# Kernel tuning notes

Hardware: AMD Instinct MI355X
Metric: run time of the kernel (lower is better)

The kernel has to match this reference:

```python
import jax, jax.numpy as jnp
import numpy as np

D = 768   # embedding_len
NL = 4    # nleft attributes
NR = 4    # nright attributes
LL = 256  # total left tokens
LR = 256  # total right tokens
DE = (NL + NR) * D  # entity-matching highway width


def setup_inputs() -> dict:
    key = jax.random.key(0)
    ks = jax.random.split(key, 12)
    f = lambda k, s: (jax.random.normal(k, s, jnp.float32) * 0.02)
    return {
        "left_emb": jax.random.normal(ks[0], (LL, D), jnp.float32),
        "right_emb": jax.random.normal(ks[1], (LR, D), jnp.float32),
        "Wn_tok": f(ks[2], (D, D)), "bn_tok": jnp.zeros((D,), jnp.float32),
        "Wg_tok": f(ks[3], (D, D)), "bg_tok": jnp.full((D,), -2.0, jnp.float32),
        "W_lin_tok": f(ks[4], (D, 1)), "b_lin_tok": jnp.zeros((1,), jnp.float32),
        "attr_emb_left": f(ks[5], (NL, D)),
        "attr_emb_right": f(ks[6], (NR, D)),
        "Wn_ent": f(ks[7], (DE, DE)), "bn_ent": jnp.zeros((DE,), jnp.float32),
        "Wg_ent": f(ks[8], (DE, DE)), "bg_ent": jnp.full((DE,), -2.0, jnp.float32),
        "W_lin_ent": f(ks[9], (DE, 2)), "b_lin_ent": jnp.zeros((2,), jnp.float32),
        "empty_attr_res": f(ks[10], (D,)),
        # per-attribute token counts; left includes an empty attribute
        "left_attrs_len": jnp.array([100, 80, 76, 0], dtype=jnp.int32),
        "right_attrs_len": jnp.array([64, 64, 64, 64], dtype=jnp.int32),
    }


def _highway(x, Wn, bn, Wg, bg):
    h = jax.nn.relu(x @ Wn + bn)
    g = jax.nn.sigmoid(x @ Wg + bg)
    return h * g + (1.0 - g) * x


def _token_matching(left, right, Wn, bn, Wg, bg, W_lin, b_lin):
    # compare_matrix: [L_left, L_right, D]
    cmp = jnp.abs(left[:, None, :] - right[None, :, :])
    hw = _highway(cmp, Wn, bn, Wg, bg)
    scores = hw @ W_lin + b_lin                     # [Ll, Lr, 1]
    # softmax over dim=1 (right tokens); only argmax is used downstream
    idx = jnp.argmax(scores[..., 0], axis=1)        # [Ll]
    return jnp.take_along_axis(cmp, idx[:, None, None], axis=1)[:, 0, :]  # [Ll, D]


def _attribute_matching(tokens, field_emb, cmp_res, lens, empty_attr):
    # ragged per-attribute softmax-weighted segment reduction
    n = field_emb.shape[0]
    L = tokens.shape[0]
    seg = jnp.repeat(jnp.arange(n), lens, total_repeat_length=L)   # [L]
    scores = jnp.einsum('ld,ld->l', tokens, field_emb[seg])        # [L]
    m = jax.ops.segment_max(scores, seg, num_segments=n)
    e = jnp.exp(scores - m[seg])
    z = jax.ops.segment_sum(e, seg, num_segments=n)
    w = e / z[seg]                                                  # softmax within segment
    reps = jax.ops.segment_sum(w[:, None] * cmp_res, seg, num_segments=n)  # [n, D]
    return jnp.where(lens[:, None] > 0, reps, empty_attr[None, :])


def reference(left_emb, right_emb, Wn_tok, bn_tok, Wg_tok, bg_tok,
              W_lin_tok, b_lin_tok, attr_emb_left, attr_emb_right,
              Wn_ent, bn_ent, Wg_ent, bg_ent, W_lin_ent, b_lin_ent,
              empty_attr_res, left_attrs_len, right_attrs_len):
    left_cmp = _token_matching(left_emb, right_emb, Wn_tok, bn_tok, Wg_tok, bg_tok,
                               W_lin_tok, b_lin_tok)
    right_cmp = _token_matching(right_emb, left_emb, Wn_tok, bn_tok, Wg_tok, bg_tok,
                                W_lin_tok, b_lin_tok)
    left_rep = _attribute_matching(left_emb, attr_emb_left, left_cmp,
                                   left_attrs_len, empty_attr_res)
    right_rep = _attribute_matching(right_emb, attr_emb_right, right_cmp,
                                    right_attrs_len, empty_attr_res)
    concat = jnp.concatenate([left_rep, right_rep], axis=0).reshape(1, -1)  # [1, DE]
    hw = _highway(concat, Wn_ent, bn_ent, Wg_ent, bg_ent)
    logits = hw @ W_lin_ent + b_lin_ent                                     # [1, 2]
    return jax.nn.softmax(logits, axis=1).flatten()                         # [2]
```

## Files before the change

### kernel.cpp

```cpp
#include <hip/hip_runtime.h>
#include <math.h>
#include <stdint.h>

#define DD 768
#define NT 256
#define DE 6144

typedef _Float16 half8 __attribute__((ext_vector_type(8)));
typedef _Float16 half4 __attribute__((ext_vector_type(4)));
typedef short short8 __attribute__((ext_vector_type(8)));
typedef float floatx4 __attribute__((ext_vector_type(4)));

__device__ __forceinline__ void async_ld16(const void* g, void* l) {
  __builtin_amdgcn_global_load_lds(
      (const __attribute__((address_space(1))) unsigned int*)g,
      (__attribute__((address_space(3))) unsigned int*)l, 16, 0, 0);
}

__global__ __launch_bounds__(256) void transpose_cvt(
    const float* __restrict__ Wn, const float* __restrict__ Wg,
    _Float16* __restrict__ WnT, _Float16* __restrict__ WgT)
{
  const float* W = blockIdx.z ? Wg : Wn;
  _Float16* WT = blockIdx.z ? WgT : WnT;
  __shared__ float tile[32][33];
  const int tx = threadIdx.x & 31, ty = threadIdx.x >> 5;
  const int d0 = blockIdx.x * 32, k0 = blockIdx.y * 32;
  #pragma unroll
  for (int p = 0; p < 4; ++p)
    tile[ty + p*8][tx] = W[(size_t)(k0 + ty + p*8)*DD + d0 + tx];
  __syncthreads();
  #pragma unroll
  for (int p = 0; p < 4; ++p) {
    const int d = d0 + ty + p*8;
    const int k = k0 + tx;
    const int idx = d*DD + (k & ~63) + ((((k >> 3) & 7) ^ (d & 7)) << 3) + (k & 7);
    WT[idx] = (_Float16)tile[tx][ty + p*8];
  }
}

__global__ __launch_bounds__(256) void cvt_lr(
    const float* __restrict__ L, const float* __restrict__ R,
    _Float16* __restrict__ Lh, _Float16* __restrict__ Rh)
{
  const float* src = blockIdx.y ? R : L;
  _Float16* dst = blockIdx.y ? Rh : Lh;
  const int o = blockIdx.x*1024 + threadIdx.x*4;
  float4 v = *(const float4*)&src[o];
  half4 h; h[0] = (_Float16)v.x; h[1] = (_Float16)v.y;
  h[2] = (_Float16)v.z; h[3] = (_Float16)v.w;
  *(half4*)&dst[o] = h;
}

__global__ __launch_bounds__(512, 2) void score_mfma(
    const _Float16* __restrict__ Lh, const _Float16* __restrict__ Rh,
    const _Float16* __restrict__ WnT, const _Float16* __restrict__ WgT,
    const float* __restrict__ bn, const float* __restrict__ bg,
    const float* __restrict__ Wl, float* __restrict__ Sp)
{
  const int dbase = blockIdx.x * 128;
  const int i     = blockIdx.y;
  const int tid   = threadIdx.x;

  __shared__ _Float16 As [2][256*64];
  __shared__ _Float16 Bns[2][128*64];
  __shared__ _Float16 Bgs[2][128*64];

  floatx4 accn[4][4] = {};
  floatx4 accg[4][4] = {};

  const int kg = tid & 7;
  const int rl = tid >> 3;

  const int lane = tid & 63;
  const int wid  = tid >> 6;
  const int wj = (wid & 3) * 64;
  const int wd = (wid >> 2) * 64;
  const int m = lane & 15;
  const int q = lane >> 4;
  const int gq8 = ((q ^ (m & 7)) << 3);

  const int drow = lane >> 3;
  const int dseg = lane & 7;

  int arow[4], brow[4];
  #pragma unroll
  for (int t4 = 0; t4 < 4; ++t4) {
    arow[t4] = (wj + t4*16 + m) * 64;
    brow[t4] = (wd + t4*16 + m) * 64;
  }

  {
    half8 l80 = *(const half8*)&Lh[i*DD + kg*8];
    #pragma unroll
    for (int tt = 0; tt < 2; ++tt) {
      const int brow0 = wid*16 + tt*8;
      async_ld16(&WnT[(size_t)(dbase + brow0 + drow)*DD + dseg*8],
                 &Bns[0][brow0*64]);
      async_ld16(&WgT[(size_t)(dbase + brow0 + drow)*DD + dseg*8],
                 &Bgs[0][brow0*64]);
    }
    #pragma unroll
    for (int rep = 0; rep < 4; ++rep) {
      const int row = rl + rep*64;
      half8 rv = *(const half8*)&Rh[(size_t)row*DD + kg*8];
      half8 dv8 = l80 - rv;
      short8 sb; __builtin_memcpy(&sb, &dv8, 16);
      sb &= (short)0x7FFF;
      *(short8*)&As[0][row*64 + ((kg ^ (row & 7)) << 3)] = sb;
    }
    __syncthreads();
  }

  for (int t = 0; t < 12; ++t) {
    const int c = t & 1;
    const _Float16* Ac  = As [c];
    const _Float16* Bnc = Bns[c];
    const _Float16* Bgc = Bgs[c];
    _Float16* An  = As [c ^ 1];
    _Float16* Bnn = Bns[c ^ 1];
    _Float16* Bgn = Bgs[c ^ 1];
    const int k0n = (t + 1) * 64;
    const bool st = (t < 11);

    half8 l8n;
    if (st) l8n = *(const half8*)&Lh[i*DD + k0n + kg*8];

    #pragma unroll
    for (int p = 0; p < 4; ++p) {
      const int jh = p >> 1, dh = p & 1;
      half8 af[2][2], bfn[2][2], bfg[2][2];
      #pragma unroll
      for (int kki = 0; kki < 2; ++kki) {
        const int ko = (kki*32) ^ gq8;
        #pragma unroll
        for (int u = 0; u < 2; ++u) {
          af [kki][u] = *(const half8*)&Ac [arow[jh*2 + u] + ko];
          bfn[kki][u] = *(const half8*)&Bnc[brow[dh*2 + u] + ko];
          bfg[kki][u] = *(const half8*)&Bgc[brow[dh*2 + u] + ko];
        }
      }
      half8 rv;
      if (st) {
        rv = *(const half8*)&Rh[(size_t)(rl + p*64)*DD + k0n + kg*8];
        const int tt = p & 1;
        const int brow0 = wid*16 + tt*8;
        if (p < 2) {
          async_ld16(&WnT[(size_t)(dbase + brow0 + drow)*DD + k0n + dseg*8],
                     &Bnn[brow0*64]);
        } else {
          async_ld16(&WgT[(size_t)(dbase + brow0 + drow)*DD + k0n + dseg*8],
                     &Bgn[brow0*64]);
        }
      }
      __builtin_amdgcn_sched_barrier(0);
      __builtin_amdgcn_s_barrier();
      __builtin_amdgcn_sched_barrier(0);
      __builtin_amdgcn_s_setprio(1);
      #pragma unroll
      for (int kki = 0; kki < 2; ++kki)
        #pragma unroll
        for (int u = 0; u < 2; ++u)
          #pragma unroll
          for (int v = 0; v < 2; ++v) {
            accn[jh*2+u][dh*2+v] = __builtin_amdgcn_mfma_f32_16x16x32_f16(
                af[kki][u], bfn[kki][v], accn[jh*2+u][dh*2+v], 0, 0, 0);
            accg[jh*2+u][dh*2+v] = __builtin_amdgcn_mfma_f32_16x16x32_f16(
                af[kki][u], bfg[kki][v], accg[jh*2+u][dh*2+v], 0, 0, 0);
          }
      __builtin_amdgcn_s_setprio(0);
      if (st) {
        const int row = rl + p*64;
        half8 dv8 = l8n - rv;
        short8 sb; __builtin_memcpy(&sb, &dv8, 16);
        sb &= (short)0x7FFF;
        *(short8*)&An[row*64 + ((kg ^ (row & 7)) << 3)] = sb;
      }
      __builtin_amdgcn_sched_barrier(0);
      __syncthreads();
    }
  }

  float bnv[4], bgv[4], wlv[4], lv[4];
  int dv[4];
  #pragma unroll
  for (int td = 0; td < 4; ++td) {
    const int d = dbase + wd + td*16 + m;
    dv[td] = d; bnv[td] = bn[d]; bgv[td] = bg[d]; wlv[td] = Wl[d];
    lv[td] = (float)Lh[i*DD + d];
  }
  const int jb = wj;
  const int plane = blockIdx.x * 2 + (wid >> 2);
  float* Sout = Sp + (size_t)plane * NT * NT + (size_t)i * NT;
  #pragma unroll
  for (int tj = 0; tj < 4; ++tj) {
    #pragma unroll
    for (int r = 0; r < 4; ++r) {
      const int j = jb + tj*16 + q*4 + r;
      float sc = 0.f;
      #pragma unroll
      for (int td = 0; td < 4; ++td) {
        const float nv = accn[tj][td][r] + bnv[td];
        const float gp = accg[tj][td][r] + bgv[td];
        const float g  = 1.f / (1.f + __expf(-gp));
        const float c  = fabsf(lv[td] - (float)Rh[(size_t)j*DD + dv[td]]);
        sc += (fmaxf(nv, 0.f)*g + (1.f - g)*c) * wlv[td];
      }
      sc += __shfl_xor(sc, 1, 16);
      sc += __shfl_xor(sc, 2, 16);
      sc += __shfl_xor(sc, 4, 16);
      sc += __shfl_xor(sc, 8, 16);
      if (m == 0) Sout[j] = sc;
    }
  }
}

__global__ __launch_bounds__(256) void argmax_attr(
    const float* __restrict__ Sp,
    int* __restrict__ idxL, int* __restrict__ idxR,
    const float* __restrict__ Lemb, const float* __restrict__ Remb,
    const float* __restrict__ AEl, const float* __restrict__ AEr,
    const int* __restrict__ lensL, const int* __restrict__ lensR,
    float* __restrict__ wS, int* __restrict__ segA)
{
  const int b = blockIdx.x;
  const int t = threadIdx.x;

  if (b < 2*NT) {
    const size_t off = (b < NT) ? ((size_t)b*NT + t) : ((size_t)t*NT + (b - NT));
    float v = 0.f;
    #pragma unroll
    for (int p = 0; p < 12; ++p) v += Sp[(size_t)p*NT*NT + off];
    int idx = t;
    #pragma unroll
    for (int mm = 1; mm < 64; mm <<= 1) {
      float ov = __shfl_xor(v, mm, 64);
      int   oi = __shfl_xor(idx, mm, 64);
      if (ov > v || (ov == v && oi < idx)) { v = ov; idx = oi; }
    }
    __shared__ float sv[4]; __shared__ int si[4];
    if ((t & 63) == 0) { sv[t>>6] = v; si[t>>6] = idx; }
    __syncthreads();
    if (t == 0) {
      #pragma unroll
      for (int w = 1; w < 4; ++w)
        if (sv[w] > v || (sv[w] == v && si[w] < idx)) { v = sv[w]; idx = si[w]; }
      if (b < NT) idxL[b] = idx; else idxR[b - NT] = idx;
    }
    return;
  }

  const int side = b - 2*NT;
  const float* tok = side ? Remb : Lemb;
  const float* AE  = side ? AEr  : AEl;
  const int* lens  = side ? lensR : lensL;
  const int c0 = lens[0], c1 = c0 + lens[1], c2 = c1 + lens[2];
  const int seg = (t < c0) ? 0 : (t < c1) ? 1 : (t < c2) ? 2 : 3;
  float s = 0.f;
  const float4* tr = (const float4*)&tok[(size_t)t*DD];
  const float4* ar = (const float4*)&AE[(size_t)seg*DD];
  for (int k = 0; k < DD/4; ++k) {
    float4 a = tr[k], bb = ar[k];
    s += a.x*bb.x + a.y*bb.y + a.z*bb.z + a.w*bb.w;
  }
  __shared__ float scS[NT]; __shared__ int segS[NT];
  __shared__ float mS[4], zS[4];
  scS[t] = s; segS[t] = seg;
  __syncthreads();
  if (t < 4) {
    float mx = -INFINITY;
    for (int u = 0; u < NT; ++u) if (segS[u] == t) mx = fmaxf(mx, scS[u]);
    mS[t] = mx;
    float z = 0.f;
    for (int u = 0; u < NT; ++u) if (segS[u] == t) z += __expf(scS[u] - mx);
    zS[t] = z;
  }
  __syncthreads();
  wS[side*NT + t] = __expf(s - mS[seg]) / zS[seg];
  segA[side*NT + t] = seg;
}

__global__ __launch_bounds__(256) void attr_reduce(
    const float* __restrict__ Lemb, const float* __restrict__ Remb,
    const int* __restrict__ lensL, const int* __restrict__ lensR,
    const int* __restrict__ idxL, const int* __restrict__ idxR,
    const float* __restrict__ wS, const int* __restrict__ segA,
    const float* __restrict__ empty, float* __restrict__ x)
{
  const int side = blockIdx.x;
  const float* tok = side ? Remb : Lemb;
  const float* oth = side ? Lemb : Remb;
  const int* lens  = side ? lensR : lensL;
  const int* idx   = side ? idxR  : idxL;
  const float* w   = wS + side*NT;
  const int* sg    = segA + side*NT;
  float* xo = x + side*4*DD;
  const int t = threadIdx.x;
  const int dl = t & 63, uq = t >> 6;
  const int d = blockIdx.y*64 + dl;
  float a0 = 0.f, a1 = 0.f, a2 = 0.f, a3 = 0.f;
  for (int u = uq*64; u < uq*64 + 64; ++u) {
    const float c = fabsf(tok[(size_t)u*DD + d] - oth[(size_t)idx[u]*DD + d]);
    const float wc = w[u] * c;
    const int s = sg[u];
    a0 += (s == 0) ? wc : 0.f;
    a1 += (s == 1) ? wc : 0.f;
    a2 += (s == 2) ? wc : 0.f;
    a3 += (s == 3) ? wc : 0.f;
  }
  __shared__ float red[4][4][64];
  red[uq][0][dl] = a0; red[uq][1][dl] = a1;
  red[uq][2][dl] = a2; red[uq][3][dl] = a3;
  __syncthreads();
  if (uq == 0) {
    #pragma unroll
    for (int s = 0; s < 4; ++s) {
      float v = red[0][s][dl] + red[1][s][dl] + red[2][s][dl] + red[3][s][dl];
      xo[s*DD + d] = (lens[s] > 0) ? v : empty[d];
    }
  }
}

__global__ __launch_bounds__(256) void ent_matvec4(
    const float* __restrict__ x,
    const float* __restrict__ Wn, const float* __restrict__ Wg,
    float* __restrict__ pn, float* __restrict__ pg)
{
  const float* W = blockIdx.z ? Wg : Wn;
  float* p = blockIdx.z ? pg : pn;
  __shared__ float xs[96];
  const int db = blockIdx.x;
  const int kb = blockIdx.y;
  const int tid = threadIdx.x;
  if (tid < 96) xs[tid] = x[kb*96 + tid];
  __syncthreads();
  const int col = db*1024 + tid*4;
  float4 a = {0.f,0.f,0.f,0.f};
  const size_t base = (size_t)kb*96*DE + col;
  #pragma unroll 8
  for (int kk = 0; kk < 96; ++kk) {
    const float xv = xs[kk];
    float4 w = *(const float4*)&W[base + (size_t)kk*DE];
    a.x = fmaf(xv, w.x, a.x); a.y = fmaf(xv, w.y, a.y);
    a.z = fmaf(xv, w.z, a.z); a.w = fmaf(xv, w.w, a.w);
  }
  *(float4*)&p[(size_t)kb*DE + col] = a;
}

__global__ __launch_bounds__(256) void ent_reduce(
    const float* __restrict__ pn, const float* __restrict__ pg,
    float* __restrict__ yn, float* __restrict__ yg)
{
  const int o = blockIdx.x*256 + threadIdx.x;
  float sn = 0.f, sg = 0.f;
  for (int kb = 0; kb < 64; ++kb) {
    sn += pn[(size_t)kb*DE + o];
    sg += pg[(size_t)kb*DE + o];
  }
  yn[o] = sn; yg[o] = sg;
}

__global__ __launch_bounds__(256) void final_kernel(
    const float* __restrict__ x, const float* __restrict__ yn,
    const float* __restrict__ yg, const float* __restrict__ bn,
    const float* __restrict__ bg, const float* __restrict__ Wl,
    const float* __restrict__ bl, float* __restrict__ out)
{
  const int tid = threadIdx.x;
  float a0 = 0.f, a1 = 0.f;
  for (int p = 0; p < DE/256; ++p) {
    int d = p*256 + tid;
    float n  = yn[d] + bn[d];
    float gp = yg[d] + bg[d];
    float h  = fmaxf(n, 0.f);
    float g  = 1.f / (1.f + __expf(-gp));
    float hw = h*g + (1.f - g)*x[d];
    a0 += hw * Wl[d*2 + 0];
    a1 += hw * Wl[d*2 + 1];
  }
  #pragma unroll
  for (int mm = 1; mm < 64; mm <<= 1) {
    a0 += __shfl_xor(a0, mm, 64);
    a1 += __shfl_xor(a1, mm, 64);
  }
  __shared__ float s0[4], s1[4];
  if ((tid & 63) == 0) { s0[tid>>6] = a0; s1[tid>>6] = a1; }
  __syncthreads();
  if (tid == 0) {
    for (int w = 1; w < 4; ++w) { a0 += s0[w]; a1 += s1[w]; }
    float l0 = a0 + bl[0], l1 = a1 + bl[1];
    float m = fmaxf(l0, l1);
    float e0 = __expf(l0 - m), e1 = __expf(l1 - m);
    out[0] = e0 / (e0 + e1);
    out[1] = e1 / (e0 + e1);
  }
}

extern "C" void kernel_launch(void* const* d_in, const int* in_sizes, int n_in,
                              void* d_out, int out_size, void* d_ws, size_t ws_size,
                              hipStream_t stream) {
  const float* Lemb   = (const float*)d_in[0];
  const float* Remb   = (const float*)d_in[1];
  const float* Wn_tok = (const float*)d_in[2];
  const float* bn_tok = (const float*)d_in[3];
  const float* Wg_tok = (const float*)d_in[4];
  const float* bg_tok = (const float*)d_in[5];
  const float* Wl_tok = (const float*)d_in[6];
  const float* AEl    = (const float*)d_in[8];
  const float* AEr    = (const float*)d_in[9];
  const float* Wn_ent = (const float*)d_in[10];
  const float* bn_ent = (const float*)d_in[11];
  const float* Wg_ent = (const float*)d_in[12];
  const float* bg_ent = (const float*)d_in[13];
  const float* Wl_ent = (const float*)d_in[14];
  const float* bl_ent = (const float*)d_in[15];
  const float* empty  = (const float*)d_in[16];
  const int*   lensL  = (const int*)d_in[17];
  const int*   lensR  = (const int*)d_in[18];

  char* ws = (char*)d_ws;
  float* Sp   = (float*)(ws + 0);
  float* pn   = (float*)(ws + 0);
  float* pg   = (float*)(ws + 1572864);
  int*  idxL  = (int*)  (ws + 3145728);
  int*  idxR  = (int*)  (ws + 3146752);
  float* x    = (float*)(ws + 3147776);
  float* yn   = (float*)(ws + 3172352);
  float* yg   = (float*)(ws + 3196928);
  float* wSm  = (float*)(ws + 3221504);
  int*  segA  = (int*)  (ws + 3223552);
  _Float16* WnT = (_Float16*)(ws + 3225600);
  _Float16* WgT = (_Float16*)(ws + 4405248);
  _Float16* Lh  = (_Float16*)(ws + 5584896);
  _Float16* Rh  = (_Float16*)(ws + 5978112);

  transpose_cvt<<<dim3(24, 24, 2), 256, 0, stream>>>(Wn_tok, Wg_tok, WnT, WgT);
  cvt_lr<<<dim3(192, 2), 256, 0, stream>>>(Lemb, Remb, Lh, Rh);
  score_mfma<<<dim3(6, 256), 512, 0, stream>>>(
      Lh, Rh, WnT, WgT, bn_tok, bg_tok, Wl_tok, Sp);
  argmax_attr<<<514, 256, 0, stream>>>(
      Sp, idxL, idxR, Lemb, Remb, AEl, AEr, lensL, lensR, wSm, segA);
  attr_reduce<<<dim3(2, 12), 256, 0, stream>>>(
      Lemb, Remb, lensL, lensR, idxL, idxR, wSm, segA, empty, x);
  ent_matvec4<<<dim3(6, 64, 2), 256, 0, stream>>>(x, Wn_ent, Wg_ent, pn, pg);
  ent_reduce<<<24, 256, 0, stream>>>(pn, pg, yn, yg);
  final_kernel<<<1, 256, 0, stream>>>(
      x, yn, yg, bn_ent, bg_ent, Wl_ent, bl_ent, (float*)d_out);
}
```

Measured before the change: 669.6 us.

## Build A operand in registers directly from global memory, drop LDS A tile

The |L_i - R_j| difference tile was previously built cooperatively into a double-buffered shared-memory array and then read back as MFMA fragments. Now each wave loads its own R rows and the L row straight from global into registers, computes the absolute difference in registers, and feeds the MFMAs directly, ping-ponging two register fragment sets. Only the weight tiles remain in LDS. This cuts LDS traffic and the per-subphase barriers, roughly halving shared memory use, at the cost of duplicated global/L2 reads of R across waves and extra register pressure.

New measurement: 1.018 ms. 1.52x slower.

```diff
diff --git a/kernel.cpp b/kernel.cpp
--- a/kernel.cpp
+++ b/kernel.cpp
@@ -62,15 +62,11 @@
   const int i     = blockIdx.y;
   const int tid   = threadIdx.x;
 
-  __shared__ _Float16 As [2][256*64];
   __shared__ _Float16 Bns[2][128*64];
   __shared__ _Float16 Bgs[2][128*64];
 
   floatx4 accn[4][4] = {};
   floatx4 accg[4][4] = {};
-
-  const int kg = tid & 7;
-  const int rl = tid >> 3;
 
   const int lane = tid & 63;
   const int wid  = tid >> 6;
@@ -83,102 +79,98 @@
   const int drow = lane >> 3;
   const int dseg = lane & 7;
 
-  int arow[4], brow[4];
-  #pragma unroll
-  for (int t4 = 0; t4 < 4; ++t4) {
-    arow[t4] = (wj + t4*16 + m) * 64;
-    brow[t4] = (wd + t4*16 + m) * 64;
-  }
-
-  {
-    half8 l80 = *(const half8*)&Lh[i*DD + kg*8];
+  int brow[4];
+  #pragma unroll
+  for (int t4 = 0; t4 < 4; ++t4) brow[t4] = (wd + t4*16 + m) * 64;
+
+  const _Float16* arow[4];
+  #pragma unroll
+  for (int t4 = 0; t4 < 4; ++t4)
+    arow[t4] = Rh + (size_t)(wj + t4*16 + m)*DD + q*8;
+  const _Float16* lrow = Lh + (size_t)i*DD + q*8;
+
+  auto stageB = [&](int k0, int c) {
     #pragma unroll
     for (int tt = 0; tt < 2; ++tt) {
       const int brow0 = wid*16 + tt*8;
-      async_ld16(&WnT[(size_t)(dbase + brow0 + drow)*DD + dseg*8],
-                 &Bns[0][brow0*64]);
-      async_ld16(&WgT[(size_t)(dbase + brow0 + drow)*DD + dseg*8],
-                 &Bgs[0][brow0*64]);
-    }
-    #pragma unroll
-    for (int rep = 0; rep < 4; ++rep) {
-      const int row = rl + rep*64;
-      half8 rv = *(const half8*)&Rh[(size_t)row*DD + kg*8];
-      half8 dv8 = l80 - rv;
-      short8 sb; __builtin_memcpy(&sb, &dv8, 16);
-      sb &= (short)0x7FFF;
-      *(short8*)&As[0][row*64 + ((kg ^ (row & 7)) << 3)] = sb;
-    }
-    __syncthreads();
-  }
-
-  for (int t = 0; t < 12; ++t) {
-    const int c = t & 1;
-    const _Float16* Ac  = As [c];
-    const _Float16* Bnc = Bns[c];
-    const _Float16* Bgc = Bgs[c];
-    _Float16* An  = As [c ^ 1];
-    _Float16* Bnn = Bns[c ^ 1];
-    _Float16* Bgn = Bgs[c ^ 1];
+      async_ld16(&WnT[(size_t)(dbase + brow0 + drow)*DD + k0 + dseg*8],
+                 &Bns[c][brow0*64]);
+      async_ld16(&WgT[(size_t)(dbase + brow0 + drow)*DD + k0 + dseg*8],
+                 &Bgs[c][brow0*64]);
+    }
+  };
+
+  auto loadA = [&](int k0, half8 (&rv)[4][2], half8 (&lh)[2]) {
+    #pragma unroll
+    for (int kki = 0; kki < 2; ++kki)
+      lh[kki] = *(const half8*)&lrow[k0 + kki*32];
+    #pragma unroll
+    for (int t4 = 0; t4 < 4; ++t4)
+      #pragma unroll
+      for (int kki = 0; kki < 2; ++kki)
+        rv[t4][kki] = *(const half8*)&arow[t4][k0 + kki*32];
+  };
+
+  auto cvtA = [&](half8 (&rv)[4][2], half8 (&lh)[2], half8 (&af)[4][2]) {
+    #pragma unroll
+    for (int t4 = 0; t4 < 4; ++t4)
+      #pragma unroll
+      for (int kki = 0; kki < 2; ++kki) {
+        half8 dv8 = lh[kki] - rv[t4][kki];
+        short8 sb; __builtin_memcpy(&sb, &dv8, 16);
+        sb &= (short)0x7FFF;
+        __builtin_memcpy(&af[t4][kki], &sb, 16);
+      }
+  };
+
+  half8 afA[4][2], afB[4][2];
+
+  auto kstep = [&](int t, int c, half8 (&afc)[4][2], half8 (&afn)[4][2]) {
+    const bool st = (t < 11);
     const int k0n = (t + 1) * 64;
-    const bool st = (t < 11);
-
-    half8 l8n;
-    if (st) l8n = *(const half8*)&Lh[i*DD + k0n + kg*8];
-
-    #pragma unroll
-    for (int p = 0; p < 4; ++p) {
-      const int jh = p >> 1, dh = p & 1;
-      half8 af[2][2], bfn[2][2], bfg[2][2];
+    half8 rvn[4][2], lhn[2];
+    if (st) {
+      stageB(k0n, c ^ 1);
+      loadA(k0n, rvn, lhn);
+    }
+    __builtin_amdgcn_sched_barrier(0);
+    __builtin_amdgcn_s_setprio(1);
+    #pragma unroll
+    for (int td = 0; td < 4; ++td) {
+      half8 bn_[2], bg_[2];
       #pragma unroll
       for (int kki = 0; kki < 2; ++kki) {
         const int ko = (kki*32) ^ gq8;
-        #pragma unroll
-        for (int u = 0; u < 2; ++u) {
-          af [kki][u] = *(const half8*)&Ac [arow[jh*2 + u] + ko];
-          bfn[kki][u] = *(const half8*)&Bnc[brow[dh*2 + u] + ko];
-          bfg[kki][u] = *(const half8*)&Bgc[brow[dh*2 + u] + ko];
-        }
+        bn_[kki] = *(const half8*)&Bns[c][brow[td] + ko];
+        bg_[kki] = *(const half8*)&Bgs[c][brow[td] + ko];
       }
-      half8 rv;
-      if (st) {
-        rv = *(const half8*)&Rh[(size_t)(rl + p*64)*DD + k0n + kg*8];
-        const int tt = p & 1;
-        const int brow0 = wid*16 + tt*8;
-        if (p < 2) {
-          async_ld16(&WnT[(size_t)(dbase + brow0 + drow)*DD + k0n + dseg*8],
-                     &Bnn[brow0*64]);
-        } else {
-          async_ld16(&WgT[(size_t)(dbase + brow0 + drow)*DD + k0n + dseg*8],
-                     &Bgn[brow0*64]);
-        }
-      }
-      __builtin_amdgcn_sched_barrier(0);
-      __builtin_amdgcn_s_barrier();
-      __builtin_amdgcn_sched_barrier(0);
-      __builtin_amdgcn_s_setprio(1);
       #pragma unroll
       for (int kki = 0; kki < 2; ++kki)
         #pragma unroll
-        for (int u = 0; u < 2; ++u)
-          #pragma unroll
-          for (int v = 0; v < 2; ++v) {
-            accn[jh*2+u][dh*2+v] = __builtin_amdgcn_mfma_f32_16x16x32_f16(
-                af[kki][u], bfn[kki][v], accn[jh*2+u][dh*2+v], 0, 0, 0);
-            accg[jh*2+u][dh*2+v] = __builtin_amdgcn_mfma_f32_16x16x32_f16(
-                af[kki][u], bfg[kki][v], accg[jh*2+u][dh*2+v], 0, 0, 0);
-          }
-      __builtin_amdgcn_s_setprio(0);
-      if (st) {
-        const int row = rl + p*64;
-        half8 dv8 = l8n - rv;
-        short8 sb; __builtin_memcpy(&sb, &dv8, 16);
-        sb &= (short)0x7FFF;
-        *(short8*)&An[row*64 + ((kg ^ (row & 7)) << 3)] = sb;
-      }
-      __builtin_amdgcn_sched_barrier(0);
-      __syncthreads();
-    }
+        for (int tj = 0; tj < 4; ++tj) {
+          accn[tj][td] = __builtin_amdgcn_mfma_f32_16x16x32_f16(
+              afc[tj][kki], bn_[kki], accn[tj][td], 0, 0, 0);
+          accg[tj][td] = __builtin_amdgcn_mfma_f32_16x16x32_f16(
+              afc[tj][kki], bg_[kki], accg[tj][td], 0, 0, 0);
+        }
+    }
+    __builtin_amdgcn_s_setprio(0);
+    if (st) cvtA(rvn, lhn, afn);
+    __builtin_amdgcn_sched_barrier(0);
+    __syncthreads();
+  };
+
+  stageB(0, 0);
+  {
+    half8 rv0[4][2], lh0[2];
+    loadA(0, rv0, lh0);
+    cvtA(rv0, lh0, afA);
+  }
+  __syncthreads();
+
+  for (int t = 0; t < 12; t += 2) {
+    kstep(t,     0, afA, afB);
+    kstep(t + 1, 1, afB, afA);
   }
 
   float bnv[4], bgv[4], wlv[4], lv[4];
```
